# Kernel optimization log

Hardware: AMD Instinct MI355X
Metric: run time of the kernel (lower is better)

## Reference

```python
import jax, jax.numpy as jnp
import numpy as np

N, C_IN, C_OUT, V = 4, 64, 64, 8192

def setup_inputs() -> dict:
    key = jax.random.key(0)
    k1, k2, k3, k4 = jax.random.split(key, 4)
    x = jax.random.normal(k1, (N, C_IN, 1, V), dtype=jnp.float32)
    A = jax.random.uniform(k2, (N, V, V), dtype=jnp.float32)
    W = jax.random.normal(k3, (C_OUT, C_IN, 1, 1), dtype=jnp.float32) * 0.05
    b = jax.random.normal(k4, (C_OUT,), dtype=jnp.float32) * 0.05
    return {"x": x, "A": A, "W": W, "b": b}

def reference(x, A, W, b):
    # nn.Conv2d with (1,1) kernel == per-position channel mixing (pointwise GEMM).
    # x: (N, C_in, 1, V) -> squeeze T dim -> (N, C_in, V)
    xs = x[:, :, 0, :]
    y = jnp.einsum('ncv,oc->nov', xs, W[:, :, 0, 0]) + b[None, :, None]  # (N, C_out, V)
    # graph aggregation with per-sample adjacency: torch.einsum('ncv,nvw->ncw', x, A)
    out = jnp.einsum('ncv,nvw->ncw', y, A)  # (N, C_out, V)
    return out, A
```

## Files before the change

### kernel.cpp

```cpp
#include <hip/hip_runtime.h>
#include <stdint.h>

#define NB 4
#define CC 64
#define VV 8192
#define WBK 128
#define KB 64
#define NCHUNK (VV / KB)

typedef float  f32x4  __attribute__((ext_vector_type(4)));
typedef uint32_t u32x2 __attribute__((ext_vector_type(2)));
typedef uint32_t u32x4 __attribute__((ext_vector_type(4)));
typedef __bf16 bf16x8 __attribute__((ext_vector_type(8)));

__device__ __forceinline__ int swz_idx(int row, int v) {
    return row * KB + ((((v >> 3) ^ row) & 7) << 3) + (v & 7);
}

__device__ __forceinline__ uint32_t pkbf(float a, float b) {
    union { __bf16 h[2]; uint32_t u; } t;
    t.h[0] = (__bf16)a; t.h[1] = (__bf16)b;
    return t.u;
}

__device__ __forceinline__ bf16x8 mkfrag(const __bf16* p, int row, int k0) {
    u32x2 lo = *(const u32x2*)(p + swz_idx(row, k0));
    u32x2 hi = *(const u32x2*)(p + swz_idx(row, k0 + 16));
    u32x4 u; u.x = lo.x; u.y = lo.y; u.z = hi.x; u.w = hi.y;
    return __builtin_bit_cast(bf16x8, u);
}

__global__ __launch_bounds__(256) void k_y(const float* __restrict__ x,
                                           const float* __restrict__ Wg,
                                           const float* __restrict__ bg,
                                           __bf16* __restrict__ yws) {
    const int n  = blockIdx.x >> 4;
    const int vp = (blockIdx.x & 15) * 256 + threadIdx.x;
    const int v  = vp * 2;
    const float* xg = x + (size_t)n * CC * VV + v;

    float ax[CC], ay[CC];
    #pragma unroll
    for (int c = 0; c < CC; ++c) { float bb = bg[c]; ax[c] = bb; ay[c] = bb; }

    for (int cp = 0; cp < CC; ++cp) {
        float xv0 = xg[(size_t)cp * VV];
        float xv1 = xg[(size_t)cp * VV + 1];
        #pragma unroll
        for (int c = 0; c < CC; ++c) {
            float w = Wg[c * CC + cp];
            ax[c] += w * xv0;
            ay[c] += w * xv1;
        }
    }
    const int t  = v >> 6;
    const int vv = v & 63;
    __bf16* ydst = yws + (size_t)(n * NCHUNK + t) * CC * KB;
    #pragma unroll
    for (int c = 0; c < CC; ++c)
        *(uint32_t*)&ydst[swz_idx(c, vv)] = pkbf(ax[c], ay[c]);
}

__global__ __launch_bounds__(512, 1) void k_main(const float* __restrict__ A,
                                                 const __bf16* __restrict__ yws,
                                                 float* __restrict__ out,
                                                 float* __restrict__ Acopy,
                                                 int skipTail) {
    __shared__ __attribute__((aligned(16))) __bf16 a_sh[2][WBK * KB];
    __shared__ __attribute__((aligned(16))) __bf16 y_sh[2][CC * KB];

    const int tid  = threadIdx.x;
    const int n    = blockIdx.x >> 6;
    const int w0   = (blockIdx.x & 63) * WBK;

    const int wl = tid & 127;
    const int vq = tid >> 7;

    const float* pA = A     + (size_t)n * VV * VV + (size_t)vq * 16 * VV + (size_t)w0 + wl;
    float*       pC = Acopy + (size_t)n * VV * VV + (size_t)vq * 16 * VV + (size_t)w0 + wl;
    const uint4* ysrc = (const uint4*)(yws + (size_t)n * NCHUNK * CC * KB);

    const int lane = tid & 63;
    const int wv   = tid >> 6;
    const int mrow = wv >> 2;
    const int ncol = wv & 3;
    const int l15  = lane & 15;
    const int kq   = (lane >> 4) * 4;
    const int crow = mrow * 32 + l15;
    const int wcol = ncol * 32 + l15;

    f32x4 acc[2][2];
    #pragma unroll
    for (int i = 0; i < 2; ++i)
        #pragma unroll
        for (int j = 0; j < 2; ++j) acc[i][j] = (f32x4){0.f, 0.f, 0.f, 0.f};

    float av[16];
    uint4 yv;

    auto stage_load = [&](int tt) {
        #pragma unroll
        for (int r = 0; r < 16; ++r)
            av[r] = pA[(size_t)(tt * KB + r) * VV];
        yv = ysrc[(size_t)tt * 512 + tid];
    };
    auto stage_write = [&](int tt, int b) {
        if (!(skipTail && n == 3 && tt >= 126)) {
            #pragma unroll
            for (int r = 0; r < 16; ++r)
                pC[(size_t)(tt * KB + r) * VV] = av[r];
        }
        #pragma unroll
        for (int m = 0; m < 4; ++m) {
            u32x2 val;
            val.x = pkbf(av[4 * m + 0], av[4 * m + 1]);
            val.y = pkbf(av[4 * m + 2], av[4 * m + 3]);
            *(u32x2*)&a_sh[b][swz_idx(wl, vq * 16 + 4 * m)] = val;
        }
        *(uint4*)&y_sh[b][tid * 8] = yv;
    };
    auto compute = [&](int b) {
        const __bf16* ysh = y_sh[b];
        const __bf16* ash = a_sh[b];
        #pragma unroll
        for (int s = 0; s < 2; ++s) {
            const int k0 = s * 32 + kq;
            bf16x8 a0 = mkfrag(ysh, crow,      k0);
            bf16x8 a1 = mkfrag(ysh, crow + 16, k0);
            bf16x8 b0 = mkfrag(ash, wcol,      k0);
            bf16x8 b1 = mkfrag(ash, wcol + 16, k0);
            acc[0][0] = __builtin_amdgcn_mfma_f32_16x16x32_bf16(a0, b0, acc[0][0], 0, 0, 0);
            acc[0][1] = __builtin_amdgcn_mfma_f32_16x16x32_bf16(a0, b1, acc[0][1], 0, 0, 0);
            acc[1][0] = __builtin_amdgcn_mfma_f32_16x16x32_bf16(a1, b0, acc[1][0], 0, 0, 0);
            acc[1][1] = __builtin_amdgcn_mfma_f32_16x16x32_bf16(a1, b1, acc[1][1], 0, 0, 0);
        }
    };

    stage_load(0);
    stage_write(0, 0);
    __syncthreads();
    for (int t = 0; t < NCHUNK; ++t) {
        if (t + 1 < NCHUNK) stage_load(t + 1);
        compute(t & 1);
        if (t + 1 < NCHUNK) stage_write(t + 1, (t + 1) & 1);
        __syncthreads();
    }

    float* po = out + ((size_t)n * CC) * VV + w0;
    #pragma unroll
    for (int mt = 0; mt < 2; ++mt)
        #pragma unroll
        for (int nt = 0; nt < 2; ++nt)
            #pragma unroll
            for (int r = 0; r < 4; ++r) {
                int c = mrow * 32 + mt * 16 + kq + r;
                int w = ncol * 32 + nt * 16 + l15;
                po[(size_t)c * VV + w] = acc[mt][nt][r];
            }
}

__global__ __launch_bounds__(256) void k_tailcopy(const float* __restrict__ A,
                                                  float* __restrict__ Acopy,
                                                  size_t baseFloats, size_t count4) {
    size_t i = (size_t)blockIdx.x * 256 + threadIdx.x;
    if (i < count4) {
        f32x4 v = *(const f32x4*)(A + baseFloats + i * 4);
        *(f32x4*)(Acopy + baseFloats + i * 4) = v;
    }
}

extern "C" void kernel_launch(void* const* d_in, const int* in_sizes, int n_in,
                              void* d_out, int out_size, void* d_ws, size_t ws_size,
                              hipStream_t stream) {
    (void)in_sizes; (void)n_in; (void)out_size;
    const float* x = (const float*)d_in[0];
    const float* A = (const float*)d_in[1];
    const float* W = (const float*)d_in[2];
    const float* b = (const float*)d_in[3];
    float* out   = (float*)d_out;
    float* Acopy = out + (size_t)NB * CC * VV;

    const size_t yElems = (size_t)NB * NCHUNK * CC * KB;
    __bf16* yws;
    int skipTail = 0;
    if (ws_size >= yElems * 2) {
        yws = (__bf16*)d_ws;
    } else {
        skipTail = 1;
        yws = (__bf16*)(Acopy + ((size_t)NB * VV * VV - yElems / 2));
    }

    hipLaunchKernelGGL(k_y,    dim3(NB * 16), dim3(256), 0, stream, x, W, b, yws);
    hipLaunchKernelGGL(k_main, dim3(NB * 64), dim3(512), 0, stream, A, yws, out, Acopy, skipTail);
    if (skipTail) {
        size_t base = (size_t)NB * VV * VV - yElems / 2;
        hipLaunchKernelGGL(k_tailcopy, dim3((unsigned)((yElems / 8 + 255) / 256)), dim3(256),
                           0, stream, A, Acopy, base, yElems / 8);
    }
}
```

Baseline: 427.9 us.

## Vectorize A loads/stores with nontemporal float4, deepen prefetch, re-split y kernel

The main kernel now reads and copies A as 128-bit nontemporal loads and stores over 4 rows per thread, instead of scalar strided loads over 16 rows. It holds two register stages so loads run two chunks ahead of compute, and it uses a custom barrier that waits only on LDS counters. The LDS swizzle gains an extra XOR term to avoid bank conflicts under the new write pattern. The y-projection kernel is re-split across 8x more blocks, each computing 16 output channels for one position, to raise occupancy. This trades higher register use for fewer memory instructions and better overlap on a bandwidth-bound 1 GB stream.

Measured after the change: 450.2 us. 1.05x slower.

```diff
diff --git a/kernel.cpp b/kernel.cpp
--- a/kernel.cpp
+++ b/kernel.cpp
@@ -14,7 +14,8 @@
 typedef __bf16 bf16x8 __attribute__((ext_vector_type(8)));
 
 __device__ __forceinline__ int swz_idx(int row, int v) {
-    return row * KB + ((((v >> 3) ^ row) & 7) << 3) + (v & 7);
+    int g = ((v >> 3) ^ row ^ (row >> 2)) & 7;
+    return row * KB + (g << 3) + (v & 7);
 }
 
 __device__ __forceinline__ uint32_t pkbf(float a, float b) {
@@ -30,35 +31,39 @@
     return __builtin_bit_cast(bf16x8, u);
 }
 
+__device__ __forceinline__ void wg_barrier() {
+    asm volatile("s_waitcnt lgkmcnt(0)" ::: "memory");
+    __builtin_amdgcn_s_barrier();
+    __builtin_amdgcn_sched_barrier(0);
+}
+
 __global__ __launch_bounds__(256) void k_y(const float* __restrict__ x,
                                            const float* __restrict__ Wg,
                                            const float* __restrict__ bg,
                                            __bf16* __restrict__ yws) {
-    const int n  = blockIdx.x >> 4;
-    const int vp = (blockIdx.x & 15) * 256 + threadIdx.x;
-    const int v  = vp * 2;
+    const int blk = blockIdx.x;
+    const int cg  = blk & 3;
+    const int vg  = (blk >> 2) * 256 + threadIdx.x;
+    const int n   = vg >> 13;
+    const int v   = vg & (VV - 1);
     const float* xg = x + (size_t)n * CC * VV + v;
 
-    float ax[CC], ay[CC];
-    #pragma unroll
-    for (int c = 0; c < CC; ++c) { float bb = bg[c]; ax[c] = bb; ay[c] = bb; }
+    float acc[16];
+    #pragma unroll
+    for (int i = 0; i < 16; ++i) acc[i] = bg[cg * 16 + i];
 
     for (int cp = 0; cp < CC; ++cp) {
-        float xv0 = xg[(size_t)cp * VV];
-        float xv1 = xg[(size_t)cp * VV + 1];
-        #pragma unroll
-        for (int c = 0; c < CC; ++c) {
-            float w = Wg[c * CC + cp];
-            ax[c] += w * xv0;
-            ay[c] += w * xv1;
-        }
+        float xv = xg[(size_t)cp * VV];
+        #pragma unroll
+        for (int i = 0; i < 16; ++i)
+            acc[i] += Wg[(cg * 16 + i) * CC + cp] * xv;
     }
     const int t  = v >> 6;
     const int vv = v & 63;
     __bf16* ydst = yws + (size_t)(n * NCHUNK + t) * CC * KB;
     #pragma unroll
-    for (int c = 0; c < CC; ++c)
-        *(uint32_t*)&ydst[swz_idx(c, vv)] = pkbf(ax[c], ay[c]);
+    for (int i = 0; i < 16; ++i)
+        ydst[swz_idx(cg * 16 + i, vv)] = (__bf16)acc[i];
 }
 
 __global__ __launch_bounds__(512, 1) void k_main(const float* __restrict__ A,
@@ -69,15 +74,15 @@
     __shared__ __attribute__((aligned(16))) __bf16 a_sh[2][WBK * KB];
     __shared__ __attribute__((aligned(16))) __bf16 y_sh[2][CC * KB];
 
-    const int tid  = threadIdx.x;
-    const int n    = blockIdx.x >> 6;
-    const int w0   = (blockIdx.x & 63) * WBK;
-
-    const int wl = tid & 127;
-    const int vq = tid >> 7;
-
-    const float* pA = A     + (size_t)n * VV * VV + (size_t)vq * 16 * VV + (size_t)w0 + wl;
-    float*       pC = Acopy + (size_t)n * VV * VV + (size_t)vq * 16 * VV + (size_t)w0 + wl;
+    const int tid = threadIdx.x;
+    const int n   = blockIdx.x >> 6;
+    const int w0  = (blockIdx.x & 63) * WBK;
+
+    const int wq = tid & 31;
+    const int rg = tid >> 5;
+
+    const float* pA = A     + (size_t)n * VV * VV + (size_t)rg * 4 * VV + w0 + 4 * wq;
+    float*       pC = Acopy + (size_t)n * VV * VV + (size_t)rg * 4 * VV + w0 + 4 * wq;
     const uint4* ysrc = (const uint4*)(yws + (size_t)n * NCHUNK * CC * KB);
 
     const int lane = tid & 63;
@@ -95,30 +100,36 @@
         #pragma unroll
         for (int j = 0; j < 2; ++j) acc[i][j] = (f32x4){0.f, 0.f, 0.f, 0.f};
 
-    float av[16];
-    uint4 yv;
-
-    auto stage_load = [&](int tt) {
-        #pragma unroll
-        for (int r = 0; r < 16; ++r)
-            av[r] = pA[(size_t)(tt * KB + r) * VV];
-        yv = ysrc[(size_t)tt * 512 + tid];
-    };
-    auto stage_write = [&](int tt, int b) {
-        if (!(skipTail && n == 3 && tt >= 126)) {
-            #pragma unroll
-            for (int r = 0; r < 16; ++r)
-                pC[(size_t)(tt * KB + r) * VV] = av[r];
-        }
-        #pragma unroll
-        for (int m = 0; m < 4; ++m) {
-            u32x2 val;
-            val.x = pkbf(av[4 * m + 0], av[4 * m + 1]);
-            val.y = pkbf(av[4 * m + 2], av[4 * m + 3]);
-            *(u32x2*)&a_sh[b][swz_idx(wl, vq * 16 + 4 * m)] = val;
-        }
-        *(uint4*)&y_sh[b][tid * 8] = yv;
-    };
+    f32x4 ra[4], rb[4];
+    uint4 yra, yrb;
+
+#define LOADT(BUF, YV, TT)                                                        \
+    do {                                                                          \
+        _Pragma("unroll")                                                         \
+        for (int i = 0; i < 4; ++i)                                               \
+            BUF[i] = __builtin_nontemporal_load(                                  \
+                (const f32x4*)(pA + (size_t)((TT) * KB + i) * VV));               \
+        YV = ysrc[(size_t)(TT) * 512 + tid];                                      \
+    } while (0)
+
+#define WRITET(BUF, YV, TT, B)                                                    \
+    do {                                                                          \
+        if (!(skipTail && n == 3 && (TT) >= 126)) {                               \
+            _Pragma("unroll")                                                     \
+            for (int i = 0; i < 4; ++i)                                           \
+                __builtin_nontemporal_store(BUF[i],                               \
+                    (f32x4*)(pC + (size_t)((TT) * KB + i) * VV));                 \
+        }                                                                         \
+        _Pragma("unroll")                                                         \
+        for (int j = 0; j < 4; ++j) {                                             \
+            u32x2 val;                                                            \
+            val.x = pkbf(BUF[0][j], BUF[1][j]);                                   \
+            val.y = pkbf(BUF[2][j], BUF[3][j]);                                   \
+            *(u32x2*)&a_sh[B][swz_idx(4 * wq + j, rg * 4)] = val;                 \
+        }                                                                         \
+        *(uint4*)&y_sh[B][tid * 8] = YV;                                          \
+    } while (0)
+
     auto compute = [&](int b) {
         const __bf16* ysh = y_sh[b];
         const __bf16* ash = a_sh[b];
@@ -136,15 +147,24 @@
         }
     };
 
-    stage_load(0);
-    stage_write(0, 0);
-    __syncthreads();
-    for (int t = 0; t < NCHUNK; ++t) {
-        if (t + 1 < NCHUNK) stage_load(t + 1);
-        compute(t & 1);
-        if (t + 1 < NCHUNK) stage_write(t + 1, (t + 1) & 1);
-        __syncthreads();
-    }
+    LOADT(ra, yra, 0);
+    LOADT(rb, yrb, 1);
+    WRITET(ra, yra, 0, 0);
+    wg_barrier();
+
+    for (int t = 0; t < NCHUNK; t += 2) {
+        if (t + 2 < NCHUNK) LOADT(ra, yra, t + 2);
+        compute(0);
+        WRITET(rb, yrb, t + 1, 1);
+        wg_barrier();
+        if (t + 3 < NCHUNK) LOADT(rb, yrb, t + 3);
+        compute(1);
+        if (t + 2 < NCHUNK) WRITET(ra, yra, t + 2, 0);
+        wg_barrier();
+    }
+
+#undef LOADT
+#undef WRITET
 
     float* po = out + ((size_t)n * CC) * VV + w0;
     #pragma unroll
@@ -190,8 +210,8 @@
         yws = (__bf16*)(Acopy + ((size_t)NB * VV * VV - yElems / 2));
     }
 
-    hipLaunchKernelGGL(k_y,    dim3(NB * 16), dim3(256), 0, stream, x, W, b, yws);
-    hipLaunchKernelGGL(k_main, dim3(NB * 64), dim3(512), 0, stream, A, yws, out, Acopy, skipTail);
+    hipLaunchKernelGGL(k_y,    dim3(NB * 128), dim3(256), 0, stream, x, W, b, yws);
+    hipLaunchKernelGGL(k_main, dim3(NB * 64),  dim3(512), 0, stream, A, yws, out, Acopy, skipTail);
     if (skipTail) {
         size_t base = (size_t)NB * VV * VV - yElems / 2;
         hipLaunchKernelGGL(k_tailcopy, dim3((unsigned)((yElems / 8 + 255) / 256)), dim3(256),
```

## Widen grids for both kernels by halving main tile width and splitting channels

Applied to the files above, without the earlier changes.

The pointwise-conv kernel is split across four channel groups per block with one vertex per thread, so it launches 512 blocks instead of 64. The main aggregation kernel halves its output column tile from 128 to 64. That doubles the block count to 512, and the launch bound now allows 4 blocks per SM. The goal is better latency hiding and CU utilisation on the bandwidth-bound stream over A. In exchange, each thread keeps fewer outstanding loads, stores to the y workspace are narrower, and each block does less MFMA work per byte of shared data.

Result: slower. 443.0 us (+3.5%).

```diff
diff --git a/kernel.cpp b/kernel.cpp
--- a/kernel.cpp
+++ b/kernel.cpp
@@ -4,7 +4,7 @@
 #define NB 4
 #define CC 64
 #define VV 8192
-#define WBK 128
+#define WBK 64
 #define KB 64
 #define NCHUNK (VV / KB)
 
@@ -34,34 +34,32 @@
                                            const float* __restrict__ Wg,
                                            const float* __restrict__ bg,
                                            __bf16* __restrict__ yws) {
-    const int n  = blockIdx.x >> 4;
-    const int vp = (blockIdx.x & 15) * 256 + threadIdx.x;
-    const int v  = vp * 2;
+    const int blk = blockIdx.x;
+    const int cg  = blk & 3;
+    const int vg  = (blk >> 2) * 256 + threadIdx.x;
+    const int n   = vg >> 13;
+    const int v   = vg & (VV - 1);
     const float* xg = x + (size_t)n * CC * VV + v;
 
-    float ax[CC], ay[CC];
+    float acc[16];
     #pragma unroll
-    for (int c = 0; c < CC; ++c) { float bb = bg[c]; ax[c] = bb; ay[c] = bb; }
+    for (int i = 0; i < 16; ++i) acc[i] = bg[cg * 16 + i];
 
     for (int cp = 0; cp < CC; ++cp) {
-        float xv0 = xg[(size_t)cp * VV];
-        float xv1 = xg[(size_t)cp * VV + 1];
+        float xv = xg[(size_t)cp * VV];
         #pragma unroll
-        for (int c = 0; c < CC; ++c) {
-            float w = Wg[c * CC + cp];
-            ax[c] += w * xv0;
-            ay[c] += w * xv1;
-        }
+        for (int i = 0; i < 16; ++i)
+            acc[i] += Wg[(cg * 16 + i) * CC + cp] * xv;
     }
     const int t  = v >> 6;
     const int vv = v & 63;
     __bf16* ydst = yws + (size_t)(n * NCHUNK + t) * CC * KB;
     #pragma unroll
-    for (int c = 0; c < CC; ++c)
-        *(uint32_t*)&ydst[swz_idx(c, vv)] = pkbf(ax[c], ay[c]);
+    for (int i = 0; i < 16; ++i)
+        ydst[swz_idx(cg * 16 + i, vv)] = (__bf16)acc[i];
 }
 
-__global__ __launch_bounds__(512, 1) void k_main(const float* __restrict__ A,
+__global__ __launch_bounds__(512, 4) void k_main(const float* __restrict__ A,
                                                  const __bf16* __restrict__ yws,
                                                  float* __restrict__ out,
                                                  float* __restrict__ Acopy,
@@ -69,15 +67,15 @@
     __shared__ __attribute__((aligned(16))) __bf16 a_sh[2][WBK * KB];
     __shared__ __attribute__((aligned(16))) __bf16 y_sh[2][CC * KB];
 
-    const int tid  = threadIdx.x;
-    const int n    = blockIdx.x >> 6;
-    const int w0   = (blockIdx.x & 63) * WBK;
+    const int tid = threadIdx.x;
+    const int n   = blockIdx.x >> 7;
+    const int w0  = (blockIdx.x & 127) * WBK;
 
-    const int wl = tid & 127;
-    const int vq = tid >> 7;
+    const int wl = tid & 63;
+    const int vq = tid >> 6;
 
-    const float* pA = A     + (size_t)n * VV * VV + (size_t)vq * 16 * VV + (size_t)w0 + wl;
-    float*       pC = Acopy + (size_t)n * VV * VV + (size_t)vq * 16 * VV + (size_t)w0 + wl;
+    const float* pA = A     + (size_t)n * VV * VV + (size_t)vq * 8 * VV + w0 + wl;
+    float*       pC = Acopy + (size_t)n * VV * VV + (size_t)vq * 8 * VV + w0 + wl;
     const uint4* ysrc = (const uint4*)(yws + (size_t)n * NCHUNK * CC * KB);
 
     const int lane = tid & 63;
@@ -87,36 +85,32 @@
     const int l15  = lane & 15;
     const int kq   = (lane >> 4) * 4;
     const int crow = mrow * 32 + l15;
-    const int wcol = ncol * 32 + l15;
+    const int wcol = ncol * 16 + l15;
 
-    f32x4 acc[2][2];
-    #pragma unroll
-    for (int i = 0; i < 2; ++i)
-        #pragma unroll
-        for (int j = 0; j < 2; ++j) acc[i][j] = (f32x4){0.f, 0.f, 0.f, 0.f};
+    f32x4 acc[2];
+    acc[0] = (f32x4){0.f, 0.f, 0.f, 0.f};
+    acc[1] = (f32x4){0.f, 0.f, 0.f, 0.f};
 
-    float av[16];
+    float av[8];
     uint4 yv;
 
     auto stage_load = [&](int tt) {
         #pragma unroll
-        for (int r = 0; r < 16; ++r)
+        for (int r = 0; r < 8; ++r)
             av[r] = pA[(size_t)(tt * KB + r) * VV];
         yv = ysrc[(size_t)tt * 512 + tid];
     };
     auto stage_write = [&](int tt, int b) {
         if (!(skipTail && n == 3 && tt >= 126)) {
             #pragma unroll
-            for (int r = 0; r < 16; ++r)
+            for (int r = 0; r < 8; ++r)
                 pC[(size_t)(tt * KB + r) * VV] = av[r];
         }
-        #pragma unroll
-        for (int m = 0; m < 4; ++m) {
-            u32x2 val;
-            val.x = pkbf(av[4 * m + 0], av[4 * m + 1]);
-            val.y = pkbf(av[4 * m + 2], av[4 * m + 3]);
-            *(u32x2*)&a_sh[b][swz_idx(wl, vq * 16 + 4 * m)] = val;
-        }
+        u32x2 v0, v1;
+        v0.x = pkbf(av[0], av[1]); v0.y = pkbf(av[2], av[3]);
+        v1.x = pkbf(av[4], av[5]); v1.y = pkbf(av[6], av[7]);
+        *(u32x2*)&a_sh[b][swz_idx(wl, vq * 8)]     = v0;
+        *(u32x2*)&a_sh[b][swz_idx(wl, vq * 8 + 4)] = v1;
         *(uint4*)&y_sh[b][tid * 8] = yv;
     };
     auto compute = [&](int b) {
@@ -128,11 +122,8 @@
             bf16x8 a0 = mkfrag(ysh, crow,      k0);
             bf16x8 a1 = mkfrag(ysh, crow + 16, k0);
             bf16x8 b0 = mkfrag(ash, wcol,      k0);
-            bf16x8 b1 = mkfrag(ash, wcol + 16, k0);
-            acc[0][0] = __builtin_amdgcn_mfma_f32_16x16x32_bf16(a0, b0, acc[0][0], 0, 0, 0);
-            acc[0][1] = __builtin_amdgcn_mfma_f32_16x16x32_bf16(a0, b1, acc[0][1], 0, 0, 0);
-            acc[1][0] = __builtin_amdgcn_mfma_f32_16x16x32_bf16(a1, b0, acc[1][0], 0, 0, 0);
-            acc[1][1] = __builtin_amdgcn_mfma_f32_16x16x32_bf16(a1, b1, acc[1][1], 0, 0, 0);
+            acc[0] = __builtin_amdgcn_mfma_f32_16x16x32_bf16(a0, b0, acc[0], 0, 0, 0);
+            acc[1] = __builtin_amdgcn_mfma_f32_16x16x32_bf16(a1, b0, acc[1], 0, 0, 0);
         }
     };
 
@@ -146,17 +137,14 @@
         __syncthreads();
     }
 
-    float* po = out + ((size_t)n * CC) * VV + w0;
+    float* po = out + (size_t)n * CC * VV + w0;
     #pragma unroll
     for (int mt = 0; mt < 2; ++mt)
         #pragma unroll
-        for (int nt = 0; nt < 2; ++nt)
-            #pragma unroll
-            for (int r = 0; r < 4; ++r) {
-                int c = mrow * 32 + mt * 16 + kq + r;
-                int w = ncol * 32 + nt * 16 + l15;
-                po[(size_t)c * VV + w] = acc[mt][nt][r];
-            }
+        for (int r = 0; r < 4; ++r) {
+            int c = mrow * 32 + mt * 16 + kq + r;
+            po[(size_t)c * VV + wcol] = acc[mt][r];
+        }
 }
 
 __global__ __launch_bounds__(256) void k_tailcopy(const float* __restrict__ A,
@@ -190,8 +178,8 @@
         yws = (__bf16*)(Acopy + ((size_t)NB * VV * VV - yElems / 2));
     }
 
-    hipLaunchKernelGGL(k_y,    dim3(NB * 16), dim3(256), 0, stream, x, W, b, yws);
-    hipLaunchKernelGGL(k_main, dim3(NB * 64), dim3(512), 0, stream, A, yws, out, Acopy, skipTail);
+    hipLaunchKernelGGL(k_y,    dim3(NB * 128), dim3(256), 0, stream, x, W, b, yws);
+    hipLaunchKernelGGL(k_main, dim3(NB * 128), dim3(512), 0, stream, A, yws, out, Acopy, skipTail);
     if (skipTail) {
         size_t base = (size_t)NB * VV * VV - yElems / 2;
         hipLaunchKernelGGL(k_tailcopy, dim3((unsigned)((yElems / 8 + 255) / 256)), dim3(256),
```

## Vectorize A loads/stores, deepen register prefetch, split y kernel across channel groups

Applied to the files above, without the earlier changes.

The main kernel now has each thread load 4 consecutive columns of A as float4 across 4 rows, instead of 16 scalar loads down one column. It keeps two register stages in flight, so global loads for chunk t+2 are issued before compute on chunk t, and the A copy-out is also vectorized. The LDS swizzle adds a row>>2 term to cut bank conflicts for the new write pattern. The y projection kernel is split into 4 channel groups, giving 4x more blocks and lower register pressure. The cost is more live registers in the main kernel and a reshuffled LDS write pattern.

Measured after the change: 382.9 us. -10.5%, faster.

```diff
diff --git a/kernel.cpp b/kernel.cpp
--- a/kernel.cpp
+++ b/kernel.cpp
@@ -8,13 +8,14 @@
 #define KB 64
 #define NCHUNK (VV / KB)
 
-typedef float  f32x4  __attribute__((ext_vector_type(4)));
+typedef float  f32x4 __attribute__((ext_vector_type(4)));
 typedef uint32_t u32x2 __attribute__((ext_vector_type(2)));
 typedef uint32_t u32x4 __attribute__((ext_vector_type(4)));
 typedef __bf16 bf16x8 __attribute__((ext_vector_type(8)));
 
 __device__ __forceinline__ int swz_idx(int row, int v) {
-    return row * KB + ((((v >> 3) ^ row) & 7) << 3) + (v & 7);
+    int g = ((v >> 3) ^ row ^ (row >> 2)) & 7;
+    return row * KB + (g << 3) + (v & 7);
 }
 
 __device__ __forceinline__ uint32_t pkbf(float a, float b) {
@@ -34,31 +35,34 @@
                                            const float* __restrict__ Wg,
                                            const float* __restrict__ bg,
                                            __bf16* __restrict__ yws) {
-    const int n  = blockIdx.x >> 4;
-    const int vp = (blockIdx.x & 15) * 256 + threadIdx.x;
-    const int v  = vp * 2;
+    const int bid  = blockIdx.x;
+    const int n    = bid >> 6;
+    const int cg   = (bid >> 4) & 3;
+    const int slab = bid & 15;
+    const int vp   = slab * 256 + threadIdx.x;
+    const int v    = vp * 2;
     const float* xg = x + (size_t)n * CC * VV + v;
 
-    float ax[CC], ay[CC];
-    #pragma unroll
-    for (int c = 0; c < CC; ++c) { float bb = bg[c]; ax[c] = bb; ay[c] = bb; }
-
+    float a0[16], a1[16];
+    #pragma unroll
+    for (int i = 0; i < 16; ++i) { float bb = bg[cg * 16 + i]; a0[i] = bb; a1[i] = bb; }
+
+    #pragma unroll 4
     for (int cp = 0; cp < CC; ++cp) {
-        float xv0 = xg[(size_t)cp * VV];
-        float xv1 = xg[(size_t)cp * VV + 1];
-        #pragma unroll
-        for (int c = 0; c < CC; ++c) {
-            float w = Wg[c * CC + cp];
-            ax[c] += w * xv0;
-            ay[c] += w * xv1;
+        float2 xv = *(const float2*)(xg + (size_t)cp * VV);
+        #pragma unroll
+        for (int i = 0; i < 16; ++i) {
+            float w = Wg[(cg * 16 + i) * CC + cp];
+            a0[i] += w * xv.x;
+            a1[i] += w * xv.y;
         }
     }
     const int t  = v >> 6;
     const int vv = v & 63;
     __bf16* ydst = yws + (size_t)(n * NCHUNK + t) * CC * KB;
     #pragma unroll
-    for (int c = 0; c < CC; ++c)
-        *(uint32_t*)&ydst[swz_idx(c, vv)] = pkbf(ax[c], ay[c]);
+    for (int i = 0; i < 16; ++i)
+        *(uint32_t*)&ydst[swz_idx(cg * 16 + i, vv)] = pkbf(a0[i], a1[i]);
 }
 
 __global__ __launch_bounds__(512, 1) void k_main(const float* __restrict__ A,
@@ -69,15 +73,15 @@
     __shared__ __attribute__((aligned(16))) __bf16 a_sh[2][WBK * KB];
     __shared__ __attribute__((aligned(16))) __bf16 y_sh[2][CC * KB];
 
-    const int tid  = threadIdx.x;
-    const int n    = blockIdx.x >> 6;
-    const int w0   = (blockIdx.x & 63) * WBK;
-
-    const int wl = tid & 127;
-    const int vq = tid >> 7;
-
-    const float* pA = A     + (size_t)n * VV * VV + (size_t)vq * 16 * VV + (size_t)w0 + wl;
-    float*       pC = Acopy + (size_t)n * VV * VV + (size_t)vq * 16 * VV + (size_t)w0 + wl;
+    const int tid = threadIdx.x;
+    const int n   = blockIdx.x >> 6;
+    const int w0  = (blockIdx.x & 63) * WBK;
+
+    const int wq = tid & 31;
+    const int rg = tid >> 5;
+
+    const float* pA = A     + (size_t)n * VV * VV + (size_t)rg * 4 * VV + w0 + 4 * wq;
+    float*       pC = Acopy + (size_t)n * VV * VV + (size_t)rg * 4 * VV + w0 + 4 * wq;
     const uint4* ysrc = (const uint4*)(yws + (size_t)n * NCHUNK * CC * KB);
 
     const int lane = tid & 63;
@@ -95,29 +99,30 @@
         #pragma unroll
         for (int j = 0; j < 2; ++j) acc[i][j] = (f32x4){0.f, 0.f, 0.f, 0.f};
 
-    float av[16];
-    uint4 yv;
-
-    auto stage_load = [&](int tt) {
-        #pragma unroll
-        for (int r = 0; r < 16; ++r)
-            av[r] = pA[(size_t)(tt * KB + r) * VV];
-        yv = ysrc[(size_t)tt * 512 + tid];
-    };
-    auto stage_write = [&](int tt, int b) {
-        if (!(skipTail && n == 3 && tt >= 126)) {
-            #pragma unroll
-            for (int r = 0; r < 16; ++r)
-                pC[(size_t)(tt * KB + r) * VV] = av[r];
+    f32x4 ra[4], rb[4];
+    uint4 yra, yrb;
+
+    auto gload = [&](f32x4 (&R)[4], uint4& Y, int tt) {
+        #pragma unroll
+        for (int i = 0; i < 4; ++i)
+            R[i] = *(const f32x4*)(pA + (size_t)(tt * KB + i) * VV);
+        Y = ysrc[(size_t)tt * 512 + tid];
+    };
+    auto gstore = [&](const f32x4 (&R)[4], int tt) {
+        if (skipTail && n == 3 && tt >= 126) return;
+        #pragma unroll
+        for (int i = 0; i < 4; ++i)
+            *(f32x4*)(pC + (size_t)(tt * KB + i) * VV) = R[i];
+    };
+    auto ldsw = [&](const f32x4 (&R)[4], const uint4& Y, int b) {
+        #pragma unroll
+        for (int j = 0; j < 4; ++j) {
+            u32x2 val;
+            val.x = pkbf(R[0][j], R[1][j]);
+            val.y = pkbf(R[2][j], R[3][j]);
+            *(u32x2*)&a_sh[b][swz_idx(4 * wq + j, rg * 4)] = val;
         }
-        #pragma unroll
-        for (int m = 0; m < 4; ++m) {
-            u32x2 val;
-            val.x = pkbf(av[4 * m + 0], av[4 * m + 1]);
-            val.y = pkbf(av[4 * m + 2], av[4 * m + 3]);
-            *(u32x2*)&a_sh[b][swz_idx(wl, vq * 16 + 4 * m)] = val;
-        }
-        *(uint4*)&y_sh[b][tid * 8] = yv;
+        *(uint4*)&y_sh[b][tid * 8] = Y;
     };
     auto compute = [&](int b) {
         const __bf16* ysh = y_sh[b];
@@ -136,17 +141,25 @@
         }
     };
 
-    stage_load(0);
-    stage_write(0, 0);
+    gload(ra, yra, 0);
+    gload(rb, yrb, 1);
+    ldsw(ra, yra, 0);
     __syncthreads();
-    for (int t = 0; t < NCHUNK; ++t) {
-        if (t + 1 < NCHUNK) stage_load(t + 1);
-        compute(t & 1);
-        if (t + 1 < NCHUNK) stage_write(t + 1, (t + 1) & 1);
+
+    for (int t = 0; t < NCHUNK; t += 2) {
+        gstore(ra, t);
+        if (t + 2 < NCHUNK) gload(ra, yra, t + 2);
+        compute(0);
+        ldsw(rb, yrb, 1);
         __syncthreads();
-    }
-
-    float* po = out + ((size_t)n * CC) * VV + w0;
+        gstore(rb, t + 1);
+        if (t + 3 < NCHUNK) gload(rb, yrb, t + 3);
+        compute(1);
+        if (t + 2 < NCHUNK) ldsw(ra, yra, 0);
+        __syncthreads();
+    }
+
+    float* po = out + (size_t)n * CC * VV + w0;
     #pragma unroll
     for (int mt = 0; mt < 2; ++mt)
         #pragma unroll
@@ -190,7 +203,7 @@
         yws = (__bf16*)(Acopy + ((size_t)NB * VV * VV - yElems / 2));
     }
 
-    hipLaunchKernelGGL(k_y,    dim3(NB * 16), dim3(256), 0, stream, x, W, b, yws);
+    hipLaunchKernelGGL(k_y,    dim3(256),     dim3(256), 0, stream, x, W, b, yws);
     hipLaunchKernelGGL(k_main, dim3(NB * 64), dim3(512), 0, stream, A, yws, out, Acopy, skipTail);
     if (skipTail) {
         size_t base = (size_t)NB * VV * VV - yElems / 2;
```
